# Performance work log

Hardware: AMD Instinct MI355X
Metric: run time of the kernel (lower is better)

## Reference

```python
import jax, jax.numpy as jnp
import numpy as np

FEATURE_HEIGHT = 50
FEATURE_WIDTH = 50


def setup_inputs() -> dict:
    key = jax.random.key(0)
    k1, k2, k3 = jax.random.split(key, 3)
    bs, K, H, D = 16, FEATURE_HEIGHT * FEATURE_WIDTH, 8, 32
    Q, L, P = 2000, 1, 4
    value = jax.random.normal(k1, (bs, K, H, D), dtype=jnp.float32)
    value_spatial_shapes = jnp.array([[FEATURE_HEIGHT, FEATURE_WIDTH]], dtype=jnp.int64)
    sampling_locations = jax.random.uniform(k2, (bs, Q, H, L, P, 2), dtype=jnp.float32)
    attention_weights = jax.random.uniform(k3, (bs, Q, H, L, P), dtype=jnp.float32)
    return {
        "value": value,
        "value_spatial_shapes": value_spatial_shapes,
        "sampling_locations": sampling_locations,
        "attention_weights": attention_weights,
    }


def _bilinear_sample(img, grid):
    """torch.F.grid_sample(mode='bilinear', padding_mode='zeros', align_corners=False).

    img:  (N, D, h, w)
    grid: (N, Q, P, 2), last dim (x, y) in [-1, 1]
    returns (N, D, Q, P)
    """
    N, D, h, w = img.shape
    # unnormalize (align_corners=False)
    x = (grid[..., 0] + 1.0) * (w * 0.5) - 0.5  # (N, Q, P)
    y = (grid[..., 1] + 1.0) * (h * 0.5) - 0.5
    x0 = jnp.floor(x)
    y0 = jnp.floor(y)
    x1 = x0 + 1.0
    y1 = y0 + 1.0
    wx1 = x - x0
    wx0 = 1.0 - wx1
    wy1 = y - y0
    wy0 = 1.0 - wy1

    img_flat = img.reshape(N, D, h * w)

    def corner(ix, iy, wgt):
        valid = ((ix >= 0) & (ix < w) & (iy >= 0) & (iy < h)).astype(img.dtype)
        ixc = jnp.clip(ix, 0, w - 1).astype(jnp.int32)
        iyc = jnp.clip(iy, 0, h - 1).astype(jnp.int32)
        idx = (iyc * w + ixc).reshape(N, -1)  # (N, Q*P)
        vals = jnp.take_along_axis(img_flat, idx[:, None, :], axis=2)  # (N, D, Q*P)
        vals = vals.reshape(N, D, *ix.shape[1:])  # (N, D, Q, P)
        return vals * (wgt * valid)[:, None]

    out = corner(x0, y0, wx0 * wy0)
    out = out + corner(x1, y0, wx1 * wy0)
    out = out + corner(x0, y1, wx0 * wy1)
    out = out + corner(x1, y1, wx1 * wy1)
    return out


def reference(value, value_spatial_shapes, sampling_locations, attention_weights):
    bs, K, H, D = value.shape
    _, Q, _, L, P, _ = sampling_locations.shape
    h, w = FEATURE_HEIGHT, FEATURE_WIDTH

    sampling_grids = 2.0 * sampling_locations - 1.0  # (bs, Q, H, L, P, 2)
    # value -> (bs*H, D, h, w)
    v = value.reshape(bs, K, H * D).transpose(0, 2, 1).reshape(bs * H, D, h, w)
    # level 0 grid -> (bs*H, Q, P, 2)
    g = jnp.transpose(sampling_grids[:, :, :, 0], (0, 2, 1, 3, 4)).reshape(bs * H, Q, P, 2)
    sampled = _bilinear_sample(v, g)  # (bs*H, D, Q, P)
    # attention weights -> (bs*H, 1, Q, L*P)
    aw = jnp.transpose(attention_weights, (0, 2, 1, 3, 4)).reshape(bs * H, 1, Q, L * P)
    out = (sampled * aw).sum(-1)  # (bs*H, D, Q)
    out = out.reshape(bs, H * D, Q).transpose(0, 2, 1)  # (bs, Q, H*D)
    return out
```

## Files before the change

kernel.cpp:

```cpp
#include <hip/hip_runtime.h>
#include <hip/hip_fp16.h>


#define FH 50
#define FW 50
#define KK (FH * FW)
#define NH 8
#define ND 32
#define NQ 2000
#define NP 4
#define QHALF 1000

__global__ __launch_bounds__(1024, 4) void deform_attn_kernel(
    const float* __restrict__ value,
    const float* __restrict__ loc,
    const float* __restrict__ attw,
    float* __restrict__ out)
{
    extern __shared__ ushort sv[];

    const int blk = blockIdx.x;
    const int xcd = blk & 7;
    const int s = blk >> 3;
    const int bph = s >> 4;
    const int h = (s >> 1) & 7;
    const int qh = s & 1;
    const int b = xcd + (bph << 3);

    {
        const float4* __restrict__ vsrc = (const float4*)value;
        const size_t vbase = (size_t)b * KK * 64 + h * 8;
        for (int i = threadIdx.x; i < KK * 8; i += 1024) {
            const int k = i >> 3;
            const int c = i & 7;
            const float4 f = vsrc[vbase + (size_t)k * 64 + c];
            const __half2 p0 = __floats2half2_rn(f.x, f.y);
            const __half2 p1 = __floats2half2_rn(f.z, f.w);
            uint2 packed;
            packed.x = *(const unsigned int*)&p0;
            packed.y = *(const unsigned int*)&p1;
            *((uint2*)&sv[(size_t)i * 4]) = packed;
        }
    }
    __syncthreads();

    const int c = threadIdx.x & 7;
    const int grp = threadIdx.x >> 3;

    const float4* __restrict__ loc4 = (const float4*)loc;
    const float4* __restrict__ attw4 = (const float4*)attw;
    float4* __restrict__ out4 = (float4*)out;

    for (int j = 0; j < 8; ++j) {
        const int ql = j * 128 + grp;
        if (ql >= QHALF) break;
        const int q = qh * QHALF + ql;
        const int gid = (b * NQ + q) * NH + h;

        const float4 l0 = loc4[(size_t)gid * 2];
        const float4 l1 = loc4[(size_t)gid * 2 + 1];
        const float4 a4 = attw4[gid];

        const float pxx[NP] = {l0.x, l0.z, l1.x, l1.z};
        const float pyy[NP] = {l0.y, l0.w, l1.y, l1.w};
        const float awp[NP] = {a4.x, a4.y, a4.z, a4.w};

        int offs[16];
        float wts[16];
#pragma unroll
        for (int p = 0; p < NP; ++p) {
            const float fx = pxx[p] * (float)FW - 0.5f;
            const float fy = pyy[p] * (float)FH - 0.5f;
            const float x0f = floorf(fx);
            const float y0f = floorf(fy);
            const int x0 = (int)x0f, y0 = (int)y0f;
            const int x1 = x0 + 1, y1 = y0 + 1;
            const float wx1 = fx - x0f, wx0 = 1.f - wx1;
            const float wy1 = fy - y0f, wy0 = 1.f - wy1;

            const bool vx0 = (x0 >= 0) & (x0 < FW);
            const bool vx1 = (x1 >= 0) & (x1 < FW);
            const bool vy0 = (y0 >= 0) & (y0 < FH);
            const bool vy1 = (y1 >= 0) & (y1 < FH);

            const int cx0 = min(max(x0, 0), FW - 1);
            const int cx1 = min(max(x1, 0), FW - 1);
            const int cy0 = min(max(y0, 0), FH - 1);
            const int cy1 = min(max(y1, 0), FH - 1);

            offs[p * 4 + 0] = (cy0 * FW + cx0) * 32 + c * 4;
            offs[p * 4 + 1] = (cy0 * FW + cx1) * 32 + c * 4;
            offs[p * 4 + 2] = (cy1 * FW + cx0) * 32 + c * 4;
            offs[p * 4 + 3] = (cy1 * FW + cx1) * 32 + c * 4;

            wts[p * 4 + 0] = ((vx0 & vy0) ? (wx0 * wy0) : 0.f) * awp[p];
            wts[p * 4 + 1] = ((vx1 & vy0) ? (wx1 * wy0) : 0.f) * awp[p];
            wts[p * 4 + 2] = ((vx0 & vy1) ? (wx0 * wy1) : 0.f) * awp[p];
            wts[p * 4 + 3] = ((vx1 & vy1) ? (wx1 * wy1) : 0.f) * awp[p];
        }

        float a0 = 0.f, a1 = 0.f, a2 = 0.f, a3 = 0.f;
#pragma unroll
        for (int i = 0; i < 16; ++i) {
            const uint2 rv = *((const uint2*)&sv[offs[i]]);
            const float w = wts[i];
            const float2 f0 = __half22float2(*(const __half2*)&rv.x);
            const float2 f1 = __half22float2(*(const __half2*)&rv.y);
            a0 += w * f0.x; a1 += w * f0.y;
            a2 += w * f1.x; a3 += w * f1.y;
        }

        out4[(size_t)(b * NQ + q) * 64 + h * 8 + c] =
            make_float4(a0, a1, a2, a3);
    }
}

extern "C" void kernel_launch(void* const* d_in, const int* in_sizes, int n_in,
                              void* d_out, int out_size, void* d_ws, size_t ws_size,
                              hipStream_t stream) {
    const float* value = (const float*)d_in[0];
    const float* loc  = (const float*)d_in[2];
    const float* attw = (const float*)d_in[3];
    float* out = (float*)d_out;

    static_assert(KK * 32 * sizeof(ushort) == 160000, "LDS size");
    hipFuncSetAttribute((const void*)deform_attn_kernel,
                        hipFuncAttributeMaxDynamicSharedMemorySize, 160000);

    deform_attn_kernel<<<256, 1024, 160000, stream>>>(value, loc, attw, out);
}
```

Before: 120.6 us.

## Split channel dimension across blocks and prefetch next query's sampling data

Each block now handles half of the 32 channels for one (batch, head, query-half), so grid doubles to 512 blocks of 512 threads with 80KB LDS instead of 160KB. This lets two blocks share a CU and halves the per-block staging load. Sampling locations and weights for the next iteration are loaded ahead, and LDS gathers are batched before the FMA loop to expose more memory parallelism. The cost is that the location/weight loads and bilinear coordinate math are duplicated across the two channel halves.

```diff
diff --git a/kernel.cpp b/kernel.cpp
--- a/kernel.cpp
+++ b/kernel.cpp
@@ -6,12 +6,11 @@
 #define FW 50
 #define KK (FH * FW)
 #define NH 8
-#define ND 32
 #define NQ 2000
 #define NP 4
 #define QHALF 1000
 
-__global__ __launch_bounds__(1024, 4) void deform_attn_kernel(
+__global__ __launch_bounds__(512, 4) void deform_attn_kernel(
     const float* __restrict__ value,
     const float* __restrict__ loc,
     const float* __restrict__ attw,
@@ -22,18 +21,19 @@
     const int blk = blockIdx.x;
     const int xcd = blk & 7;
     const int s = blk >> 3;
-    const int bph = s >> 4;
-    const int h = (s >> 1) & 7;
-    const int qh = s & 1;
+    const int h = s & 7;
+    const int chalf = (s >> 3) & 1;
+    const int qh = (s >> 4) & 1;
+    const int bph = (s >> 5) & 1;
     const int b = xcd + (bph << 3);
 
     {
         const float4* __restrict__ vsrc = (const float4*)value;
-        const size_t vbase = (size_t)b * KK * 64 + h * 8;
-        for (int i = threadIdx.x; i < KK * 8; i += 1024) {
-            const int k = i >> 3;
-            const int c = i & 7;
-            const float4 f = vsrc[vbase + (size_t)k * 64 + c];
+        const size_t vbase = (size_t)b * KK * 64 + h * 8 + chalf * 4;
+        for (int i = threadIdx.x; i < KK * 4; i += 512) {
+            const int k = i >> 2;
+            const int cc = i & 3;
+            const float4 f = vsrc[vbase + (size_t)k * 64 + cc];
             const __half2 p0 = __floats2half2_rn(f.x, f.y);
             const __half2 p1 = __floats2half2_rn(f.z, f.w);
             uint2 packed;
@@ -44,26 +44,37 @@
     }
     __syncthreads();
 
-    const int c = threadIdx.x & 7;
-    const int grp = threadIdx.x >> 3;
+    const int c = threadIdx.x & 3;
+    const int grp = threadIdx.x >> 2;
 
     const float4* __restrict__ loc4 = (const float4*)loc;
     const float4* __restrict__ attw4 = (const float4*)attw;
     float4* __restrict__ out4 = (float4*)out;
 
+    int qn = qh * QHALF + grp;
+    int gidn = (b * NQ + qn) * NH + h;
+    float4 l0 = loc4[(size_t)gidn * 2];
+    float4 l1 = loc4[(size_t)gidn * 2 + 1];
+    float4 a4 = attw4[gidn];
+    int qcur = qn;
+
+#pragma unroll 2
     for (int j = 0; j < 8; ++j) {
-        const int ql = j * 128 + grp;
-        if (ql >= QHALF) break;
-        const int q = qh * QHALF + ql;
-        const int gid = (b * NQ + q) * NH + h;
+        const float4 c0 = l0, c1 = l1, ca = a4;
+        const int q = qcur;
+        if (j < 7) {
+            const int qln = min((j + 1) * 128 + grp, QHALF - 1);
+            qn = qh * QHALF + qln;
+            gidn = (b * NQ + qn) * NH + h;
+            l0 = loc4[(size_t)gidn * 2];
+            l1 = loc4[(size_t)gidn * 2 + 1];
+            a4 = attw4[gidn];
+            qcur = qn;
+        }
 
-        const float4 l0 = loc4[(size_t)gid * 2];
-        const float4 l1 = loc4[(size_t)gid * 2 + 1];
-        const float4 a4 = attw4[gid];
-
-        const float pxx[NP] = {l0.x, l0.z, l1.x, l1.z};
-        const float pyy[NP] = {l0.y, l0.w, l1.y, l1.w};
-        const float awp[NP] = {a4.x, a4.y, a4.z, a4.w};
+        const float pxx[NP] = {c0.x, c0.z, c1.x, c1.z};
+        const float pyy[NP] = {c0.y, c0.w, c1.y, c1.w};
+        const float awp[NP] = {ca.x, ca.y, ca.z, ca.w};
 
         int offs[16];
         float wts[16];
@@ -88,10 +99,10 @@
             const int cy0 = min(max(y0, 0), FH - 1);
             const int cy1 = min(max(y1, 0), FH - 1);
 
-            offs[p * 4 + 0] = (cy0 * FW + cx0) * 32 + c * 4;
-            offs[p * 4 + 1] = (cy0 * FW + cx1) * 32 + c * 4;
-            offs[p * 4 + 2] = (cy1 * FW + cx0) * 32 + c * 4;
-            offs[p * 4 + 3] = (cy1 * FW + cx1) * 32 + c * 4;
+            offs[p * 4 + 0] = (cy0 * FW + cx0) * 16 + c * 4;
+            offs[p * 4 + 1] = (cy0 * FW + cx1) * 16 + c * 4;
+            offs[p * 4 + 2] = (cy1 * FW + cx0) * 16 + c * 4;
+            offs[p * 4 + 3] = (cy1 * FW + cx1) * 16 + c * 4;
 
             wts[p * 4 + 0] = ((vx0 & vy0) ? (wx0 * wy0) : 0.f) * awp[p];
             wts[p * 4 + 1] = ((vx1 & vy0) ? (wx1 * wy0) : 0.f) * awp[p];
@@ -99,19 +110,23 @@
             wts[p * 4 + 3] = ((vx1 & vy1) ? (wx1 * wy1) : 0.f) * awp[p];
         }
 
-        float a0 = 0.f, a1 = 0.f, a2 = 0.f, a3 = 0.f;
+        uint2 u[16];
+#pragma unroll
+        for (int i = 0; i < 16; ++i)
+            u[i] = *((const uint2*)&sv[offs[i]]);
+
+        float2 a01 = {0.f, 0.f}, a23 = {0.f, 0.f};
 #pragma unroll
         for (int i = 0; i < 16; ++i) {
-            const uint2 rv = *((const uint2*)&sv[offs[i]]);
             const float w = wts[i];
-            const float2 f0 = __half22float2(*(const __half2*)&rv.x);
-            const float2 f1 = __half22float2(*(const __half2*)&rv.y);
-            a0 += w * f0.x; a1 += w * f0.y;
-            a2 += w * f1.x; a3 += w * f1.y;
+            const float2 f0 = __half22float2(*(const __half2*)&u[i].x);
+            const float2 f1 = __half22float2(*(const __half2*)&u[i].y);
+            a01.x += w * f0.x; a01.y += w * f0.y;
+            a23.x += w * f1.x; a23.y += w * f1.y;
         }
 
-        out4[(size_t)(b * NQ + q) * 64 + h * 8 + c] =
-            make_float4(a0, a1, a2, a3);
+        out4[(size_t)(b * NQ + q) * 64 + h * 8 + chalf * 4 + c] =
+            make_float4(a01.x, a01.y, a23.x, a23.y);
     }
 }
 
@@ -123,9 +138,8 @@
     const float* attw = (const float*)d_in[3];
     float* out = (float*)d_out;
 
-    static_assert(KK * 32 * sizeof(ushort) == 160000, "LDS size");
     hipFuncSetAttribute((const void*)deform_attn_kernel,
-                        hipFuncAttributeMaxDynamicSharedMemorySize, 160000);
+                        hipFuncAttributeMaxDynamicSharedMemorySize, 80000);
 
-    deform_attn_kernel<<<256, 1024, 160000, stream>>>(value, loc, attw, out);
+    deform_attn_kernel<<<512, 512, 80000, stream>>>(value, loc, attw, out);
 }
```

Measured after the change: 119.6 us. About the same (-0.8%).
